# Kernel tuning notes

Hardware: AMD Instinct MI355X
Metric: run time of the kernel (lower is better)

## Reference

```python
import jax, jax.numpy as jnp
import numpy as np


def setup_inputs() -> dict:
    key = jax.random.key(0)
    kq, kk, kv = jax.random.split(key, 3)
    shape = (2, 8, 1024, 64)  # [B, H, L, D]
    return {
        "q": jax.random.normal(kq, shape, dtype=jnp.float32),
        "k": jax.random.normal(kk, shape, dtype=jnp.float32),
        "v": jax.random.normal(kv, shape, dtype=jnp.float32),
    }


def reference(q, k, v):
    B, H, L, D = q.shape
    eps = 1e-6
    q = jax.nn.relu(q).reshape(B * H, L, D)
    k = jax.nn.relu(k).reshape(B * H, L, D)
    v = jax.nn.relu(v).reshape(B * H, L, D)

    # cosFormer positional reweighting: pi/2 * (i+1)/L
    idx = (jnp.pi / 2) * jnp.arange(1, L + 1, dtype=q.dtype) / L  # [L]
    s = jnp.sin(idx)[None, :, None]  # [1, L, 1]
    c = jnp.cos(idx)[None, :, None]

    q_ = jnp.concatenate([q * s, q * c], axis=-1)  # [N, L, 2D]
    k_ = jnp.concatenate([k * s, k * c], axis=-1)  # [N, L, 2D]

    # causal linear attention via cumulative kv outer product
    kv = jnp.einsum("nld,nlm->nldm", k_, v)        # [N, L, 2D, D]
    kv_cum = jnp.cumsum(kv, axis=1)                  # [N, L, 2D, D]
    qkv = jnp.einsum("nld,nldm->nlm", q_, kv_cum)  # [N, L, D]

    k_cum = jnp.cumsum(k_, axis=1)                   # [N, L, 2D]
    denom = jnp.clip(jnp.einsum("nld,nld->nl", q_, k_cum), eps, None)

    out = qkv / denom[..., None]
    return out.reshape(B, H, L, D)
```

## Files before the change

kernel.cpp:

```cpp
#include <hip/hip_runtime.h>
#include <hip/hip_fp16.h>

#define N_HEADS 16
#define L_SEQ   1024
#define D_HEAD  64
#define D2      128
#define T_CHUNK 32
#define N_CHUNK (L_SEQ / T_CHUNK)
#define KV_ELEMS (D2 * D_HEAD)
#define PK_UINTS (KV_ELEMS / 2)

#define ROWP 140
#define PARTP 132

__device__ __forceinline__ int pad_col(int d2) { return d2 + 4 * (d2 >> 5); }

#define SINCOS_SCALE 1.53398078788564122971e-3f

__device__ __forceinline__ unsigned int packh2(float a, float b) {
    __half2 h = __floats2half2_rn(a, b);
    return __builtin_bit_cast(unsigned int, h);
}
__device__ __forceinline__ float2 unpackh2(unsigned int u) {
    __half2 h = __builtin_bit_cast(__half2, u);
    return __half22float2(h);
}

__device__ __forceinline__ float red8_dpp(float x) {
    x += __int_as_float(__builtin_amdgcn_mov_dpp(__float_as_int(x), 0xB1, 0xF, 0xF, true));
    x += __int_as_float(__builtin_amdgcn_mov_dpp(__float_as_int(x), 0x4E, 0xF, 0xF, true));
    x += __int_as_float(__builtin_amdgcn_mov_dpp(__float_as_int(x), 0x141, 0xF, 0xF, true));
    return x;
}

__global__ __launch_bounds__(256, 2) void k1_chunk_sums(
    const float* __restrict__ k, const float* __restrict__ v,
    unsigned int* __restrict__ sumkv, float* __restrict__ sumk)
{
    __shared__ __attribute__((aligned(16))) float k_s[T_CHUNK][ROWP];
    __shared__ __attribute__((aligned(16))) float v_s[T_CHUNK][D_HEAD];
    __shared__ float s_tab[T_CHUNK], c_tab[T_CHUNK];

    const int c = blockIdx.x, n = blockIdx.y;
    const int tid = threadIdx.x;
    const int base = (n * L_SEQ + c * T_CHUNK) * D_HEAD;

    if (tid < T_CHUNK) {
        float th = SINCOS_SCALE * (float)(c * T_CHUNK + tid + 1);
        s_tab[tid] = __sinf(th);
        c_tab[tid] = __cosf(th);
    }
    __syncthreads();

    const float4* k4g = (const float4*)(k + base);
    const float4* v4g = (const float4*)(v + base);
#pragma unroll
    for (int j = 0; j < 2; ++j) {
        int i4 = j * 256 + tid;
        int l = i4 >> 4, d = (i4 & 15) << 2;
        float4 kk = k4g[i4], vv = v4g[i4];
        kk.x = fmaxf(kk.x, 0.f); kk.y = fmaxf(kk.y, 0.f);
        kk.z = fmaxf(kk.z, 0.f); kk.w = fmaxf(kk.w, 0.f);
        vv.x = fmaxf(vv.x, 0.f); vv.y = fmaxf(vv.y, 0.f);
        vv.z = fmaxf(vv.z, 0.f); vv.w = fmaxf(vv.w, 0.f);
        float s = s_tab[l], cs = c_tab[l];
        *(float4*)&k_s[l][pad_col(d)]      = make_float4(kk.x*s,  kk.y*s,  kk.z*s,  kk.w*s);
        *(float4*)&k_s[l][pad_col(d + 64)] = make_float4(kk.x*cs, kk.y*cs, kk.z*cs, kk.w*cs);
        *(float4*)&v_s[l][d] = vv;
    }
    __syncthreads();

    if (tid < D2) {
        int pc = pad_col(tid);
        float ks = 0.f;
#pragma unroll
        for (int l = 0; l < T_CHUNK; ++l) ks += k_s[l][pc];
        sumk[(n * N_CHUNK + c) * D2 + tid] = ks;
    }

    const int g = tid & 7, mh = (tid >> 3) << 1;
    const int gbase = pad_col(16 * g);

    float st0[16], st1[16];
#pragma unroll
    for (int j = 0; j < 16; ++j) { st0[j] = 0.f; st1[j] = 0.f; }

    for (int l = 0; l < T_CHUNK; ++l) {
        float2 vm = *(const float2*)&v_s[l][mh];
        const float4* kv4 = (const float4*)&k_s[l][gbase];
#pragma unroll
        for (int jj = 0; jj < 4; ++jj) {
            float4 kk = kv4[jj];
            st0[4*jj+0] = fmaf(kk.x, vm.x, st0[4*jj+0]);
            st1[4*jj+0] = fmaf(kk.x, vm.y, st1[4*jj+0]);
            st0[4*jj+1] = fmaf(kk.y, vm.x, st0[4*jj+1]);
            st1[4*jj+1] = fmaf(kk.y, vm.y, st1[4*jj+1]);
            st0[4*jj+2] = fmaf(kk.z, vm.x, st0[4*jj+2]);
            st1[4*jj+2] = fmaf(kk.z, vm.y, st1[4*jj+2]);
            st0[4*jj+3] = fmaf(kk.w, vm.x, st0[4*jj+3]);
            st1[4*jj+3] = fmaf(kk.w, vm.y, st1[4*jj+3]);
        }
    }

    uint4* dst = (uint4*)(sumkv + (size_t)(n * N_CHUNK + c) * PK_UINTS);
    dst[0*256 + tid] = make_uint4(packh2(st0[0],st0[1]),  packh2(st0[2],st0[3]),
                                  packh2(st0[4],st0[5]),  packh2(st0[6],st0[7]));
    dst[1*256 + tid] = make_uint4(packh2(st0[8],st0[9]),  packh2(st0[10],st0[11]),
                                  packh2(st0[12],st0[13]),packh2(st0[14],st0[15]));
    dst[2*256 + tid] = make_uint4(packh2(st1[0],st1[1]),  packh2(st1[2],st1[3]),
                                  packh2(st1[4],st1[5]),  packh2(st1[6],st1[7]));
    dst[3*256 + tid] = make_uint4(packh2(st1[8],st1[9]),  packh2(st1[10],st1[11]),
                                  packh2(st1[12],st1[13]),packh2(st1[14],st1[15]));
}

__global__ __launch_bounds__(256) void k2_prefix(
    unsigned int* __restrict__ sumkv, float* __restrict__ sumk)
{
    const int x = blockIdx.x, n = blockIdx.y;
    const int tid = threadIdx.x;

    if (x < 8) {
        uint2* base = (uint2*)(sumkv + (size_t)n * N_CHUNK * PK_UINTS) + x * 256 + tid;
        uint2 t[N_CHUNK];
#pragma unroll
        for (int c = 0; c < N_CHUNK; ++c) t[c] = base[c * (PK_UINTS / 2)];
        float r0 = 0.f, r1 = 0.f, r2 = 0.f, r3 = 0.f;
#pragma unroll
        for (int c = 0; c < N_CHUNK; ++c) {
            uint2 cur = t[c];
            base[c * (PK_UINTS / 2)] = make_uint2(packh2(r0, r1), packh2(r2, r3));
            float2 lo = unpackh2(cur.x), hi = unpackh2(cur.y);
            r0 += lo.x; r1 += lo.y; r2 += hi.x; r3 += hi.y;
        }
    } else if (tid < D2) {
        float* bk = sumk + n * N_CHUNK * D2 + tid;
        float t[N_CHUNK];
#pragma unroll
        for (int c = 0; c < N_CHUNK; ++c) t[c] = bk[c * D2];
        float r = 0.f;
#pragma unroll
        for (int c = 0; c < N_CHUNK; ++c) { bk[c * D2] = r; r += t[c]; }
    }
}

__global__ __launch_bounds__(256, 2) void k3_output(
    const float* __restrict__ q, const float* __restrict__ k,
    const float* __restrict__ v, const unsigned int* __restrict__ sumkv,
    const float* __restrict__ sumk, float* __restrict__ out)
{
    __shared__ __attribute__((aligned(16))) float k_s[T_CHUNK][ROWP];
    __shared__ __attribute__((aligned(16))) float q_s[T_CHUNK][ROWP];
    __shared__ __attribute__((aligned(16))) float v_s[T_CHUNK][D_HEAD];
    __shared__ __attribute__((aligned(16))) float pool[T_CHUNK * PARTP];
    __shared__ float rden_s[T_CHUNK];
    __shared__ float s_tab[T_CHUNK], c_tab[T_CHUNK];

    float (*part_s)[PARTP] = (float(*)[PARTP])pool;
    float (*out_s)[D_HEAD] = (float(*)[D_HEAD])pool;

    const int c = blockIdx.x, n = blockIdx.y;
    const int tid = threadIdx.x;
    const int base = (n * L_SEQ + c * T_CHUNK) * D_HEAD;

    if (tid < T_CHUNK) {
        float th = SINCOS_SCALE * (float)(c * T_CHUNK + tid + 1);
        s_tab[tid] = __sinf(th);
        c_tab[tid] = __cosf(th);
    }
    __syncthreads();

    const float4* q4g = (const float4*)(q + base);
    const float4* k4g = (const float4*)(k + base);
    const float4* v4g = (const float4*)(v + base);
#pragma unroll
    for (int j = 0; j < 2; ++j) {
        int i4 = j * 256 + tid;
        int l = i4 >> 4, d = (i4 & 15) << 2;
        float4 kk = k4g[i4], qq = q4g[i4], vv = v4g[i4];
        kk.x = fmaxf(kk.x, 0.f); kk.y = fmaxf(kk.y, 0.f);
        kk.z = fmaxf(kk.z, 0.f); kk.w = fmaxf(kk.w, 0.f);
        qq.x = fmaxf(qq.x, 0.f); qq.y = fmaxf(qq.y, 0.f);
        qq.z = fmaxf(qq.z, 0.f); qq.w = fmaxf(qq.w, 0.f);
        vv.x = fmaxf(vv.x, 0.f); vv.y = fmaxf(vv.y, 0.f);
        vv.z = fmaxf(vv.z, 0.f); vv.w = fmaxf(vv.w, 0.f);
        float s = s_tab[l], cs = c_tab[l];
        *(float4*)&k_s[l][pad_col(d)]      = make_float4(kk.x*s,  kk.y*s,  kk.z*s,  kk.w*s);
        *(float4*)&k_s[l][pad_col(d + 64)] = make_float4(kk.x*cs, kk.y*cs, kk.z*cs, kk.w*cs);
        *(float4*)&q_s[l][pad_col(d)]      = make_float4(qq.x*s,  qq.y*s,  qq.z*s,  qq.w*s);
        *(float4*)&q_s[l][pad_col(d + 64)] = make_float4(qq.x*cs, qq.y*cs, qq.z*cs, qq.w*cs);
        *(float4*)&v_s[l][d] = vv;
    }

    const uint4* pkv = (const uint4*)(sumkv + (size_t)(n * N_CHUNK + c) * PK_UINTS);
    uint4 p0 = pkv[0*256 + tid];
    uint4 p1 = pkv[1*256 + tid];
    uint4 p2 = pkv[2*256 + tid];
    uint4 p3 = pkv[3*256 + tid];
    float kc = 0.f;
    if (tid < D2) kc = sumk[(n * N_CHUNK + c) * D2 + tid];

    float st0[16], st1[16];
    {
        float2 f;
        f = unpackh2(p0.x); st0[0]=f.x;  st0[1]=f.y;
        f = unpackh2(p0.y); st0[2]=f.x;  st0[3]=f.y;
        f = unpackh2(p0.z); st0[4]=f.x;  st0[5]=f.y;
        f = unpackh2(p0.w); st0[6]=f.x;  st0[7]=f.y;
        f = unpackh2(p1.x); st0[8]=f.x;  st0[9]=f.y;
        f = unpackh2(p1.y); st0[10]=f.x; st0[11]=f.y;
        f = unpackh2(p1.z); st0[12]=f.x; st0[13]=f.y;
        f = unpackh2(p1.w); st0[14]=f.x; st0[15]=f.y;
        f = unpackh2(p2.x); st1[0]=f.x;  st1[1]=f.y;
        f = unpackh2(p2.y); st1[2]=f.x;  st1[3]=f.y;
        f = unpackh2(p2.z); st1[4]=f.x;  st1[5]=f.y;
        f = unpackh2(p2.w); st1[6]=f.x;  st1[7]=f.y;
        f = unpackh2(p3.x); st1[8]=f.x;  st1[9]=f.y;
        f = unpackh2(p3.y); st1[10]=f.x; st1[11]=f.y;
        f = unpackh2(p3.z); st1[12]=f.x; st1[13]=f.y;
        f = unpackh2(p3.w); st1[14]=f.x; st1[15]=f.y;
    }

    __syncthreads();

    if (tid < D2) {
        int pc = pad_col(tid);
#pragma unroll
        for (int l = 0; l < T_CHUNK; ++l) {
            kc += k_s[l][pc];
            part_s[l][tid] = q_s[l][pc] * kc;
        }
    }
    __syncthreads();

    {
        int l = tid >> 3, j = tid & 7;
        const float4* p4 = (const float4*)&part_s[l][j * 16];
        float4 aa = p4[0], bb = p4[1], cc4 = p4[2], dd = p4[3];
        float sum = ((aa.x + aa.y) + (aa.z + aa.w)) + ((bb.x + bb.y) + (bb.z + bb.w))
                  + ((cc4.x + cc4.y) + (cc4.z + cc4.w)) + ((dd.x + dd.y) + (dd.z + dd.w));
        sum = red8_dpp(sum);
        if (j == 0) rden_s[l] = 1.f / fmaxf(sum, 1e-6f);
    }
    __syncthreads();

    const int g = tid & 7, mh = (tid >> 3) << 1;
    const int gbase = pad_col(16 * g);

    for (int l = 0; l < T_CHUNK; ++l) {
        float2 vm = *(const float2*)&v_s[l][mh];
        const float4* kv4 = (const float4*)&k_s[l][gbase];
        const float4* qv4 = (const float4*)&q_s[l][gbase];
        float a0 = 0.f, a1 = 0.f;
#pragma unroll
        for (int jj = 0; jj < 4; ++jj) {
            float4 kk = kv4[jj];
            float4 qq = qv4[jj];
            st0[4*jj+0] = fmaf(kk.x, vm.x, st0[4*jj+0]); a0 = fmaf(qq.x, st0[4*jj+0], a0);
            st1[4*jj+0] = fmaf(kk.x, vm.y, st1[4*jj+0]); a1 = fmaf(qq.x, st1[4*jj+0], a1);
            st0[4*jj+1] = fmaf(kk.y, vm.x, st0[4*jj+1]); a0 = fmaf(qq.y, st0[4*jj+1], a0);
            st1[4*jj+1] = fmaf(kk.y, vm.y, st1[4*jj+1]); a1 = fmaf(qq.y, st1[4*jj+1], a1);
            st0[4*jj+2] = fmaf(kk.z, vm.x, st0[4*jj+2]); a0 = fmaf(qq.z, st0[4*jj+2], a0);
            st1[4*jj+2] = fmaf(kk.z, vm.y, st1[4*jj+2]); a1 = fmaf(qq.z, st1[4*jj+2], a1);
            st0[4*jj+3] = fmaf(kk.w, vm.x, st0[4*jj+3]); a0 = fmaf(qq.w, st0[4*jj+3], a0);
            st1[4*jj+3] = fmaf(kk.w, vm.y, st1[4*jj+3]); a1 = fmaf(qq.w, st1[4*jj+3], a1);
        }
        a0 = red8_dpp(a0);
        a1 = red8_dpp(a1);
        if (g == 0) {
            float r = rden_s[l];
            *(float2*)&out_s[l][mh] = make_float2(a0 * r, a1 * r);
        }
    }
    __syncthreads();

    {
        float4* o4 = (float4*)(out + base);
        const float4* s4o = (const float4*)&out_s[0][0];
        o4[tid] = s4o[tid];
        o4[256 + tid] = s4o[256 + tid];
    }
}

extern "C" void kernel_launch(void* const* d_in, const int* in_sizes, int n_in,
                              void* d_out, int out_size, void* d_ws, size_t ws_size,
                              hipStream_t stream) {
    (void)in_sizes; (void)n_in; (void)out_size; (void)ws_size;
    const float* q = (const float*)d_in[0];
    const float* k = (const float*)d_in[1];
    const float* v = (const float*)d_in[2];
    float* out = (float*)d_out;

    unsigned int* sumkv = (unsigned int*)d_ws;
    float* sumk = (float*)(sumkv + (size_t)N_HEADS * N_CHUNK * PK_UINTS);

    dim3 grid(N_CHUNK, N_HEADS);
    k1_chunk_sums<<<grid, 256, 0, stream>>>(k, v, sumkv, sumk);
    dim3 grid2(9, N_HEADS);
    k2_prefix<<<grid2, 256, 0, stream>>>(sumkv, sumk);
    k3_output<<<grid, 256, 0, stream>>>(q, k, v, sumkv, sumk, out);
}
```

Baseline: 87.41 us.

## Compute output kernel intra-chunk attention with fp16 MFMA matrix products

```diff
diff --git a/kernel.cpp b/kernel.cpp
--- a/kernel.cpp
+++ b/kernel.cpp
@@ -11,11 +11,21 @@
 #define PK_UINTS (KV_ELEMS / 2)
 
 #define ROWP 140
-#define PARTP 132
-
 __device__ __forceinline__ int pad_col(int d2) { return d2 + 4 * (d2 >> 5); }
 
+#define PQ 132
+#define PS 136
+#define PV 36
+
 #define SINCOS_SCALE 1.53398078788564122971e-3f
+
+typedef _Float16 f16_t;
+typedef __attribute__((ext_vector_type(4))) _Float16 f16x4;
+typedef __attribute__((ext_vector_type(4))) float f32x4;
+
+__device__ __forceinline__ f32x4 mfma16(f16x4 a, f16x4 b, f32x4 c) {
+    return __builtin_amdgcn_mfma_f32_16x16x16f16(a, b, c, 0, 0, 0);
+}
 
 __device__ __forceinline__ unsigned int packh2(float a, float b) {
     __half2 h = __floats2half2_rn(a, b);
@@ -30,6 +40,13 @@
     x += __int_as_float(__builtin_amdgcn_mov_dpp(__float_as_int(x), 0xB1, 0xF, 0xF, true));
     x += __int_as_float(__builtin_amdgcn_mov_dpp(__float_as_int(x), 0x4E, 0xF, 0xF, true));
     x += __int_as_float(__builtin_amdgcn_mov_dpp(__float_as_int(x), 0x141, 0xF, 0xF, true));
+    return x;
+}
+__device__ __forceinline__ float red16_dpp(float x) {
+    x += __int_as_float(__builtin_amdgcn_mov_dpp(__float_as_int(x), 0xB1, 0xF, 0xF, true));
+    x += __int_as_float(__builtin_amdgcn_mov_dpp(__float_as_int(x), 0x4E, 0xF, 0xF, true));
+    x += __int_as_float(__builtin_amdgcn_mov_dpp(__float_as_int(x), 0x141, 0xF, 0xF, true));
+    x += __int_as_float(__builtin_amdgcn_mov_dpp(__float_as_int(x), 0x140, 0xF, 0xF, true));
     return x;
 }
 
@@ -103,14 +120,18 @@
     }
 
     uint4* dst = (uint4*)(sumkv + (size_t)(n * N_CHUNK + c) * PK_UINTS);
-    dst[0*256 + tid] = make_uint4(packh2(st0[0],st0[1]),  packh2(st0[2],st0[3]),
-                                  packh2(st0[4],st0[5]),  packh2(st0[6],st0[7]));
-    dst[1*256 + tid] = make_uint4(packh2(st0[8],st0[9]),  packh2(st0[10],st0[11]),
-                                  packh2(st0[12],st0[13]),packh2(st0[14],st0[15]));
-    dst[2*256 + tid] = make_uint4(packh2(st1[0],st1[1]),  packh2(st1[2],st1[3]),
-                                  packh2(st1[4],st1[5]),  packh2(st1[6],st1[7]));
-    dst[3*256 + tid] = make_uint4(packh2(st1[8],st1[9]),  packh2(st1[10],st1[11]),
-                                  packh2(st1[12],st1[13]),packh2(st1[14],st1[15]));
+    {
+        int i0 = mh * 16 + (g << 1);
+        int i1 = i0 + 16;
+        dst[i0]     = make_uint4(packh2(st0[0],st0[1]),   packh2(st0[2],st0[3]),
+                                 packh2(st0[4],st0[5]),   packh2(st0[6],st0[7]));
+        dst[i0 + 1] = make_uint4(packh2(st0[8],st0[9]),   packh2(st0[10],st0[11]),
+                                 packh2(st0[12],st0[13]), packh2(st0[14],st0[15]));
+        dst[i1]     = make_uint4(packh2(st1[0],st1[1]),   packh2(st1[2],st1[3]),
+                                 packh2(st1[4],st1[5]),   packh2(st1[6],st1[7]));
+        dst[i1 + 1] = make_uint4(packh2(st1[8],st1[9]),   packh2(st1[10],st1[11]),
+                                 packh2(st1[12],st1[13]), packh2(st1[14],st1[15]));
+    }
 }
 
 __global__ __launch_bounds__(256) void k2_prefix(
@@ -148,15 +169,14 @@
     const float* __restrict__ v, const unsigned int* __restrict__ sumkv,
     const float* __restrict__ sumk, float* __restrict__ out)
 {
-    __shared__ __attribute__((aligned(16))) float k_s[T_CHUNK][ROWP];
-    __shared__ __attribute__((aligned(16))) float q_s[T_CHUNK][ROWP];
-    __shared__ __attribute__((aligned(16))) float v_s[T_CHUNK][D_HEAD];
-    __shared__ __attribute__((aligned(16))) float pool[T_CHUNK * PARTP];
-    __shared__ float rden_s[T_CHUNK];
+    __shared__ __attribute__((aligned(16))) f16_t q16[T_CHUNK][PQ];
+    __shared__ __attribute__((aligned(16))) f16_t k16[T_CHUNK][PQ];
+    __shared__ __attribute__((aligned(16))) f16_t vt[D_HEAD][PV];
+    __shared__ __attribute__((aligned(16))) f16_t s0t[D_HEAD][PS];
+    __shared__ __attribute__((aligned(16))) f16_t pmat[T_CHUNK][PV];
+    __shared__ float kc0[D2];
+    __shared__ float den0_s[T_CHUNK], dpA[T_CHUNK], dpB[T_CHUNK], rden[T_CHUNK];
     __shared__ float s_tab[T_CHUNK], c_tab[T_CHUNK];
-
-    float (*part_s)[PARTP] = (float(*)[PARTP])pool;
-    float (*out_s)[D_HEAD] = (float(*)[D_HEAD])pool;
 
     const int c = blockIdx.x, n = blockIdx.y;
     const int tid = threadIdx.x;
@@ -184,100 +204,103 @@
         vv.x = fmaxf(vv.x, 0.f); vv.y = fmaxf(vv.y, 0.f);
         vv.z = fmaxf(vv.z, 0.f); vv.w = fmaxf(vv.w, 0.f);
         float s = s_tab[l], cs = c_tab[l];
-        *(float4*)&k_s[l][pad_col(d)]      = make_float4(kk.x*s,  kk.y*s,  kk.z*s,  kk.w*s);
-        *(float4*)&k_s[l][pad_col(d + 64)] = make_float4(kk.x*cs, kk.y*cs, kk.z*cs, kk.w*cs);
-        *(float4*)&q_s[l][pad_col(d)]      = make_float4(qq.x*s,  qq.y*s,  qq.z*s,  qq.w*s);
-        *(float4*)&q_s[l][pad_col(d + 64)] = make_float4(qq.x*cs, qq.y*cs, qq.z*cs, qq.w*cs);
-        *(float4*)&v_s[l][d] = vv;
-    }
-
-    const uint4* pkv = (const uint4*)(sumkv + (size_t)(n * N_CHUNK + c) * PK_UINTS);
-    uint4 p0 = pkv[0*256 + tid];
-    uint4 p1 = pkv[1*256 + tid];
-    uint4 p2 = pkv[2*256 + tid];
-    uint4 p3 = pkv[3*256 + tid];
-    float kc = 0.f;
-    if (tid < D2) kc = sumk[(n * N_CHUNK + c) * D2 + tid];
-
-    float st0[16], st1[16];
+        q16[l][d+0]    = (f16_t)(qq.x*s);  q16[l][d+1]    = (f16_t)(qq.y*s);
+        q16[l][d+2]    = (f16_t)(qq.z*s);  q16[l][d+3]    = (f16_t)(qq.w*s);
+        q16[l][d+64]   = (f16_t)(qq.x*cs); q16[l][d+65]   = (f16_t)(qq.y*cs);
+        q16[l][d+66]   = (f16_t)(qq.z*cs); q16[l][d+67]   = (f16_t)(qq.w*cs);
+        k16[l][d+0]    = (f16_t)(kk.x*s);  k16[l][d+1]    = (f16_t)(kk.y*s);
+        k16[l][d+2]    = (f16_t)(kk.z*s);  k16[l][d+3]    = (f16_t)(kk.w*s);
+        k16[l][d+64]   = (f16_t)(kk.x*cs); k16[l][d+65]   = (f16_t)(kk.y*cs);
+        k16[l][d+66]   = (f16_t)(kk.z*cs); k16[l][d+67]   = (f16_t)(kk.w*cs);
+        vt[d+0][l] = (f16_t)vv.x; vt[d+1][l] = (f16_t)vv.y;
+        vt[d+2][l] = (f16_t)vv.z; vt[d+3][l] = (f16_t)vv.w;
+    }
     {
-        float2 f;
-        f = unpackh2(p0.x); st0[0]=f.x;  st0[1]=f.y;
-        f = unpackh2(p0.y); st0[2]=f.x;  st0[3]=f.y;
-        f = unpackh2(p0.z); st0[4]=f.x;  st0[5]=f.y;
-        f = unpackh2(p0.w); st0[6]=f.x;  st0[7]=f.y;
-        f = unpackh2(p1.x); st0[8]=f.x;  st0[9]=f.y;
-        f = unpackh2(p1.y); st0[10]=f.x; st0[11]=f.y;
-        f = unpackh2(p1.z); st0[12]=f.x; st0[13]=f.y;
-        f = unpackh2(p1.w); st0[14]=f.x; st0[15]=f.y;
-        f = unpackh2(p2.x); st1[0]=f.x;  st1[1]=f.y;
-        f = unpackh2(p2.y); st1[2]=f.x;  st1[3]=f.y;
-        f = unpackh2(p2.z); st1[4]=f.x;  st1[5]=f.y;
-        f = unpackh2(p2.w); st1[6]=f.x;  st1[7]=f.y;
-        f = unpackh2(p3.x); st1[8]=f.x;  st1[9]=f.y;
-        f = unpackh2(p3.y); st1[10]=f.x; st1[11]=f.y;
-        f = unpackh2(p3.z); st1[12]=f.x; st1[13]=f.y;
-        f = unpackh2(p3.w); st1[14]=f.x; st1[15]=f.y;
-    }
-
-    __syncthreads();
-
-    if (tid < D2) {
-        int pc = pad_col(tid);
-#pragma unroll
-        for (int l = 0; l < T_CHUNK; ++l) {
-            kc += k_s[l][pc];
-            part_s[l][tid] = q_s[l][pc] * kc;
-        }
-    }
+        const uint4* pkv = (const uint4*)(sumkv + (size_t)(n * N_CHUNK + c) * PK_UINTS);
+#pragma unroll
+        for (int jj = 0; jj < 4; ++jj) {
+            int u = jj * 256 + tid;
+            int pos = u << 3;
+            *(uint4*)&s0t[pos >> 7][pos & 127] = pkv[u];
+        }
+    }
+    if (tid < D2) kc0[tid] = sumk[(n * N_CHUNK + c) * D2 + tid];
     __syncthreads();
 
     {
-        int l = tid >> 3, j = tid & 7;
-        const float4* p4 = (const float4*)&part_s[l][j * 16];
-        float4 aa = p4[0], bb = p4[1], cc4 = p4[2], dd = p4[3];
-        float sum = ((aa.x + aa.y) + (aa.z + aa.w)) + ((bb.x + bb.y) + (bb.z + bb.w))
-                  + ((cc4.x + cc4.y) + (cc4.z + cc4.w)) + ((dd.x + dd.y) + (dd.z + dd.w));
-        sum = red8_dpp(sum);
-        if (j == 0) rden_s[l] = 1.f / fmaxf(sum, 1e-6f);
-    }
-    __syncthreads();
-
-    const int g = tid & 7, mh = (tid >> 3) << 1;
-    const int gbase = pad_col(16 * g);
-
-    for (int l = 0; l < T_CHUNK; ++l) {
-        float2 vm = *(const float2*)&v_s[l][mh];
-        const float4* kv4 = (const float4*)&k_s[l][gbase];
-        const float4* qv4 = (const float4*)&q_s[l][gbase];
-        float a0 = 0.f, a1 = 0.f;
-#pragma unroll
-        for (int jj = 0; jj < 4; ++jj) {
-            float4 kk = kv4[jj];
-            float4 qq = qv4[jj];
-            st0[4*jj+0] = fmaf(kk.x, vm.x, st0[4*jj+0]); a0 = fmaf(qq.x, st0[4*jj+0], a0);
-            st1[4*jj+0] = fmaf(kk.x, vm.y, st1[4*jj+0]); a1 = fmaf(qq.x, st1[4*jj+0], a1);
-            st0[4*jj+1] = fmaf(kk.y, vm.x, st0[4*jj+1]); a0 = fmaf(qq.y, st0[4*jj+1], a0);
-            st1[4*jj+1] = fmaf(kk.y, vm.y, st1[4*jj+1]); a1 = fmaf(qq.y, st1[4*jj+1], a1);
-            st0[4*jj+2] = fmaf(kk.z, vm.x, st0[4*jj+2]); a0 = fmaf(qq.z, st0[4*jj+2], a0);
-            st1[4*jj+2] = fmaf(kk.z, vm.y, st1[4*jj+2]); a1 = fmaf(qq.z, st1[4*jj+2], a1);
-            st0[4*jj+3] = fmaf(kk.w, vm.x, st0[4*jj+3]); a0 = fmaf(qq.w, st0[4*jj+3], a0);
-            st1[4*jj+3] = fmaf(kk.w, vm.y, st1[4*jj+3]); a1 = fmaf(qq.w, st1[4*jj+3], a1);
-        }
-        a0 = red8_dpp(a0);
-        a1 = red8_dpp(a1);
-        if (g == 0) {
-            float r = rden_s[l];
-            *(float2*)&out_s[l][mh] = make_float2(a0 * r, a1 * r);
-        }
-    }
-    __syncthreads();
-
-    {
-        float4* o4 = (float4*)(out + base);
-        const float4* s4o = (const float4*)&out_s[0][0];
-        o4[tid] = s4o[tid];
-        o4[256 + tid] = s4o[256 + tid];
+        int l = tid >> 3, seg = (tid & 7) << 4;
+        float a = 0.f;
+#pragma unroll
+        for (int i = 0; i < 16; ++i) a += (float)q16[l][seg + i] * kc0[seg + i];
+        a = red8_dpp(a);
+        if ((tid & 7) == 0) den0_s[l] = a;
+    }
+
+    const int wave = tid >> 6, lane = tid & 63;
+    const int fr = lane & 15;
+    const int fk = (lane >> 4) << 2;
+    const int rowq = (lane >> 4) << 2;
+
+    if (wave < 3) {
+        const int mt = (wave == 0) ? 0 : 1;
+        const int nt = (wave == 2) ? 1 : 0;
+        f32x4 sa = {0.f, 0.f, 0.f, 0.f};
+#pragma unroll
+        for (int ks = 0; ks < 8; ++ks) {
+            f16x4 a = *(const f16x4*)&q16[mt * 16 + fr][ks * 16 + fk];
+            f16x4 b = *(const f16x4*)&k16[nt * 16 + fr][ks * 16 + fk];
+            sa = mfma16(a, b, sa);
+        }
+#pragma unroll
+        for (int r = 0; r < 4; ++r) {
+            int row = rowq + r;
+            float mv = (mt > nt || fr <= row) ? sa[r] : 0.f;
+            pmat[mt * 16 + row][nt * 16 + fr] = (f16_t)mv;
+            float rs = red16_dpp(mv);
+            if (fr == 0) {
+                if (wave == 2) dpB[16 + row] = rs;
+                else dpA[mt * 16 + row] = rs;
+            }
+        }
+    } else {
+        int row = lane >> 2, colb = 16 + ((lane & 3) << 2);
+        *(uint2*)&pmat[row][colb] = make_uint2(0u, 0u);
+    }
+    __syncthreads();
+
+    if (tid < T_CHUNK) {
+        float den = den0_s[tid] + dpA[tid] + ((tid >= 16) ? dpB[tid] : 0.f);
+        rden[tid] = 1.f / fmaxf(den, 1e-6f);
+    }
+
+    const int mt = wave >> 1;
+    const int nt0 = (wave & 1) << 1, nt1 = nt0 + 1;
+    f32x4 o0 = {0.f, 0.f, 0.f, 0.f}, o1 = {0.f, 0.f, 0.f, 0.f};
+#pragma unroll
+    for (int ks = 0; ks < 8; ++ks) {
+        f16x4 a  = *(const f16x4*)&q16[mt * 16 + fr][ks * 16 + fk];
+        f16x4 b0 = *(const f16x4*)&s0t[nt0 * 16 + fr][ks * 16 + fk];
+        f16x4 b1 = *(const f16x4*)&s0t[nt1 * 16 + fr][ks * 16 + fk];
+        o0 = mfma16(a, b0, o0);
+        o1 = mfma16(a, b1, o1);
+    }
+#pragma unroll
+    for (int ks = 0; ks < 2; ++ks) {
+        f16x4 a  = *(const f16x4*)&pmat[mt * 16 + fr][ks * 16 + fk];
+        f16x4 b0 = *(const f16x4*)&vt[nt0 * 16 + fr][ks * 16 + fk];
+        f16x4 b1 = *(const f16x4*)&vt[nt1 * 16 + fr][ks * 16 + fk];
+        o0 = mfma16(a, b0, o0);
+        o1 = mfma16(a, b1, o1);
+    }
+    __syncthreads();
+
+    float* og = out + base;
+#pragma unroll
+    for (int r = 0; r < 4; ++r) {
+        int row = mt * 16 + rowq + r;
+        float rd = rden[row];
+        og[row * D_HEAD + nt0 * 16 + fr] = o0[r] * rd;
+        og[row * D_HEAD + nt1 * 16 + fr] = o1[r] * rd;
     }
 }
 
```

New measurement: 79.03 us. -9.6%, faster.
